# Performance work log

Hardware: AMD Instinct MI355X
Metric: run time of the kernel (lower is better)

Reference implementation:

```python
import jax, jax.numpy as jnp
import numpy as np

DEG = 3
KNOTS = np.array([i / 9.0 for i in range(1, 9)], dtype=np.float32)  # 8 knots in (0,1)
SDIM = DEG + 1 + len(KNOTS)  # 12
B, D_IN, D_HID, D_OUT = 32768, 256, 256, 1


def spline_basis(t):
    # TruncatedPowerBasis: [1, t, t^2, t^3, relu(t-k)^3 ...]  -> (B, SDIM)
    powers = t[:, None] ** jnp.arange(DEG + 1, dtype=t.dtype)
    knots = jnp.asarray(KNOTS, dtype=t.dtype)
    spl = jax.nn.relu(t[:, None] - knots[None, :]) ** DEG
    return jnp.concatenate([powers, spl], axis=1)


def vc_layer(x, basis, W, b, in_dim, out_dim):
    # Mathematically identical to torch: W_b = basis @ W (viewed (in,out)); out = x @ W_b + basis @ b
    # Factored to avoid materializing the (B, in, out) per-sample weight tensor.
    Ws = W.reshape(SDIM, in_dim, out_dim)
    tmp = jnp.einsum('bi,sio->bso', x, Ws)        # (B, SDIM, out)
    return jnp.einsum('bs,bso->bo', basis, tmp) + basis @ b


def setup_inputs() -> dict:
    key = jax.random.key(0)
    ks = jax.random.split(key, 8)
    xavier = lambda k, shape: jax.random.uniform(
        k, shape, dtype=jnp.float32,
        minval=-1.0, maxval=1.0) * np.sqrt(6.0 / (shape[0] + shape[1]))
    return {
        'treatment': jax.random.uniform(ks[0], (B,), dtype=jnp.float32),
        'features': jax.random.normal(ks[1], (B, D_IN), dtype=jnp.float32),
        'W0': xavier(ks[2], (SDIM, D_IN * D_HID)),
        'b0': xavier(ks[3], (SDIM, D_HID)),
        'W1': xavier(ks[4], (SDIM, D_HID * D_HID)),
        'b1': xavier(ks[5], (SDIM, D_HID)),
        'W2': xavier(ks[6], (SDIM, D_HID * D_OUT)),
        'b2': xavier(ks[7], (SDIM, D_OUT)),
    }


def reference(treatment, features, W0, b0, W1, b1, W2, b2):
    basis = spline_basis(treatment)                     # (B, SDIM)
    x = vc_layer(features, basis, W0, b0, D_IN, D_HID)
    x = jax.nn.relu(x)
    x = vc_layer(x, basis, W1, b1, D_HID, D_HID)
    x = jax.nn.relu(x)
    x = vc_layer(x, basis, W2, b2, D_HID, D_OUT)        # (B, 1)
    return x
```

## Files before the change

### kernel.cpp

```cpp
#include <hip/hip_runtime.h>


typedef __attribute__((ext_vector_type(8))) _Float16 half8;
typedef __attribute__((ext_vector_type(4))) _Float16 half4;
typedef __attribute__((ext_vector_type(4))) float floatx4;

#define XPAD 264

__device__ __forceinline__ void gload16(const _Float16* g, _Float16* l){
  __builtin_amdgcn_global_load_lds(
      (const __attribute__((address_space(1))) void*)g,
      (__attribute__((address_space(3))) void*)l, 16, 0, 0);
}

__device__ __forceinline__ void stage_b(const _Float16* wt, _Float16* slot,
                                        int w, int l){
  gload16(wt +        w * 512 + l * 8, slot +        w * 512);
  gload16(wt + 4096 + w * 512 + l * 8, slot + 4096 + w * 512);
}

__device__ __forceinline__ void make_basis(float t, float* p){
  p[0] = 1.f; p[1] = t; p[2] = t*t; p[3] = p[2]*t;
  const float knots[8] = {1.f/9.f, 2.f/9.f, 3.f/9.f, 4.f/9.f,
                          5.f/9.f, 6.f/9.f, 7.f/9.f, 8.f/9.f};
  #pragma unroll
  for (int j = 0; j < 8; ++j){
    float d = t - knots[j];
    d = fmaxf(d, 0.f);
    p[4+j] = d*d*d;
  }
}

__global__ __launch_bounds__(256)
void pack_w_kernel(const float* __restrict__ W0, const float* __restrict__ W1,
                   _Float16* __restrict__ Wp0, _Float16* __restrict__ Wp1){
  __shared__ float wl[32 * 260];
  const int blk = blockIdx.x;
  const float* W = (blk < 96) ? W0 : W1;
  _Float16* Wp   = (blk < 96) ? Wp0 : Wp1;
  const int c    = (blk < 96) ? blk : blk - 96;
  const int tid  = threadIdx.x;
  const float* src = W + (size_t)c * 8192;
  #pragma unroll
  for (int it = 0; it < 8; ++it){
    int idx = it * 256 + tid;
    int r = idx >> 6, c4 = idx & 63;
    float4 v = *(const float4*)(src + (size_t)idx * 4);
    float* d = &wl[r * 260 + c4 * 4];
    d[0] = v.x; d[1] = v.y; d[2] = v.z; d[3] = v.w;
  }
  __syncthreads();
  const int tpos = (c & 7) * 12 + (c >> 3);
  _Float16* dst = Wp + (size_t)tpos * 8192;
  #pragma unroll
  for (int w = 0; w < 4; ++w){
    int v = w * 256 + tid;
    int n16 = v & 15, qq = (v >> 4) & 3, ntg = v >> 6;
    half8 o;
    #pragma unroll
    for (int j = 0; j < 8; ++j)
      o[j] = (_Float16)wl[(qq * 8 + j) * 260 + ntg * 16 + n16];
    *(half8*)(dst + (size_t)v * 8) = o;
  }
}

__device__ __forceinline__ void gemm_kloop(const _Float16* Xl, _Float16* Bl,
                                           const float* bldsT,
                                           const _Float16* __restrict__ wp,
                                           unsigned xbase, int wm, int wn,
                                           int l16, int w, int l,
                                           floatx4 acc[4][4]){
  const unsigned bbase = (unsigned)(wn * 2048 + l * 8);
  half8 xc[4], xn[4], bc[4], bn[4];
  stage_b(wp + 2 * 8192, Bl + 2 * 8192, w, l);
  #pragma unroll
  for (int nt = 0; nt < 4; ++nt)
    bc[nt] = *(const half8*)(Bl + bbase + nt * 512);
  #pragma unroll
  for (int mt = 0; mt < 4; ++mt)
    xc[mt] = *(const half8*)&Xl[xbase + mt * 16 * XPAD];
  floatx4 btc = *(const floatx4*)&bldsT[wm * 64 + l16 * 4];

  for (int ko = 0; ko < 8; ++ko){
    #pragma unroll
    for (int s = 0; s < 12; ++s){
      __asm__ __volatile__("s_waitcnt vmcnt(2)" ::: "memory");
      __builtin_amdgcn_sched_barrier(0);
      __builtin_amdgcn_s_barrier();
      __builtin_amdgcn_sched_barrier(0);

      #pragma unroll
      for (int nt = 0; nt < 4; ++nt)
        bn[nt] = *(const half8*)(Bl + ((s + 1) & 3) * 8192 + bbase + nt * 512);
      const int sn = (s == 11) ? 0 : s + 1;
      floatx4 btn = *(const floatx4*)&bldsT[sn * 128 + wm * 64 + l16 * 4];
      if (s == 0){
        const int kon = (ko + 1) & 7;
        #pragma unroll
        for (int mt = 0; mt < 4; ++mt)
          xn[mt] = *(const half8*)&Xl[xbase + kon * 32 + mt * 16 * XPAD];
      }

      _Float16 bh[4];
      #pragma unroll
      for (int mt = 0; mt < 4; ++mt) bh[mt] = (_Float16)btc[mt];
      half8 az[4];
      #pragma unroll
      for (int mt = 0; mt < 4; ++mt) az[mt] = xc[mt] * bh[mt];
      #pragma unroll
      for (int mt = 0; mt < 4; ++mt)
        #pragma unroll
        for (int nt = 0; nt < 4; ++nt)
          acc[mt][nt] = __builtin_amdgcn_mfma_f32_16x16x32_f16(
              az[mt], bc[nt], acc[mt][nt], 0, 0, 0);

      #pragma unroll
      for (int nt = 0; nt < 4; ++nt) bc[nt] = bn[nt];
      btc = btn;
      if (s == 11){
        #pragma unroll
        for (int mt = 0; mt < 4; ++mt) xc[mt] = xn[mt];
      }
      stage_b(wp + (size_t)(ko * 12 + s + 3) * 8192,
              Bl + ((s + 3) & 3) * 8192, w, l);
    }
  }
}

__device__ __forceinline__ void add_bias(const float* blds, const float* __restrict__ bias,
                                         int wm, int wn, int q, int l16,
                                         floatx4 acc[4][4]){
  for (int s = 0; s < 12; ++s){
    float bl[4];
    #pragma unroll
    for (int nt = 0; nt < 4; ++nt)
      bl[nt] = bias[s * 256 + wn * 64 + nt * 16 + l16];
    floatx4 bs[4];
    #pragma unroll
    for (int mt = 0; mt < 4; ++mt)
      bs[mt] = *(const floatx4*)&blds[s * 128 + wm * 64 + mt * 16 + q * 4];
    #pragma unroll
    for (int mt = 0; mt < 4; ++mt)
      #pragma unroll
      for (int nt = 0; nt < 4; ++nt)
        #pragma unroll
        for (int r = 0; r < 4; ++r)
          acc[mt][nt][r] += bs[mt][r] * bl[nt];
  }
}

__device__ __forceinline__ void scatter_to_xl(_Float16* Xl, floatx4 acc[4][4],
                                              int wm, int wn, int q, int l16){
  #pragma unroll
  for (int mt = 0; mt < 4; ++mt)
    #pragma unroll
    for (int nt = 0; nt < 4; ++nt)
      #pragma unroll
      for (int r = 0; r < 4; ++r)
        Xl[(wm * 64 + mt * 16 + q * 4 + r) * XPAD + wn * 64 + nt * 16 + l16] =
            (_Float16)fmaxf(acc[mt][nt][r], 0.f);
}

__global__ __launch_bounds__(512, 2)
void fused_layers_kernel(const float* __restrict__ feat, const float* __restrict__ treat,
                         const _Float16* __restrict__ Wp0, const float* __restrict__ b0,
                         const _Float16* __restrict__ Wp1, const float* __restrict__ b1,
                         _Float16* __restrict__ X2){
  __shared__ _Float16 Xl[128 * XPAD];
  __shared__ _Float16 Bl[4 * 8192];
  __shared__ float blds[12 * 128];
  __shared__ float bldsT[12 * 128];

  const int tid  = threadIdx.x;
  const int m0   = blockIdx.x * 128;
  const int lane = tid & 63;
  const int wid  = tid >> 6;
  const int wm   = wid >> 2;
  const int wn   = wid & 3;
  const int q    = lane >> 4;
  const int l16  = lane & 15;

  stage_b(Wp0,        Bl,        wid, lane);
  stage_b(Wp0 + 8192, Bl + 8192, wid, lane);

  #pragma unroll
  for (int it = 0; it < 16; ++it){
    int idx = it * 512 + tid;
    int m = idx >> 6, c = idx & 63;
    float4 v = *(const float4*)(feat + (size_t)(m0 + m) * 256 + c * 4);
    half4 h = { (_Float16)v.x, (_Float16)v.y, (_Float16)v.z, (_Float16)v.w };
    *(half4*)&Xl[m * XPAD + c * 4] = h;
  }
  if (tid < 128){
    float t = treat[m0 + tid];
    float p[12]; make_basis(t, p);
    const int r   = tid;
    const int tmt = (r >> 4) & 3;
    const int tl  = r & 15;
    const int twm = r >> 6;
    #pragma unroll
    for (int s = 0; s < 12; ++s){
      blds [s * 128 + r] = p[s];
      bldsT[s * 128 + twm * 64 + tl * 4 + tmt] = p[s];
    }
  }
  __syncthreads();

  const unsigned xbase = (unsigned)(wm * 64 + l16) * XPAD + q * 8;

  const floatx4 zero = {0.f, 0.f, 0.f, 0.f};
  floatx4 acc[4][4];
  #pragma unroll
  for (int mt = 0; mt < 4; ++mt)
    #pragma unroll
    for (int nt = 0; nt < 4; ++nt) acc[mt][nt] = zero;

  gemm_kloop(Xl, Bl, bldsT, Wp0, xbase, wm, wn, l16, wid, lane, acc);
  add_bias(blds, b0, wm, wn, q, l16, acc);
  __syncthreads();
  scatter_to_xl(Xl, acc, wm, wn, q, l16);
  stage_b(Wp1,        Bl,        wid, lane);
  stage_b(Wp1 + 8192, Bl + 8192, wid, lane);
  __syncthreads();

  #pragma unroll
  for (int mt = 0; mt < 4; ++mt)
    #pragma unroll
    for (int nt = 0; nt < 4; ++nt) acc[mt][nt] = zero;
  gemm_kloop(Xl, Bl, bldsT, Wp1, xbase, wm, wn, l16, wid, lane, acc);
  add_bias(blds, b1, wm, wn, q, l16, acc);

  __syncthreads();
  scatter_to_xl(Xl, acc, wm, wn, q, l16);
  __syncthreads();
  #pragma unroll
  for (int it = 0; it < 8; ++it){
    int idx = it * 512 + tid;
    int m = idx >> 5, c = idx & 31;
    half8 v = *(const half8*)&Xl[m * XPAD + c * 8];
    *(half8*)(X2 + (size_t)(m0 + m) * 256 + c * 8) = v;
  }
}

__global__ __launch_bounds__(256)
void final_kernel(const _Float16* __restrict__ X2, const float* __restrict__ treat,
                  const float* __restrict__ W2, const float* __restrict__ b2,
                  float* __restrict__ out){
  __shared__ float w2l[12 * 256];
  __shared__ float b2l[12];
  const int tid = threadIdx.x;
  const int m0 = blockIdx.x * 16;
  #pragma unroll
  for (int it = 0; it < 12; ++it) w2l[it * 256 + tid] = W2[it * 256 + tid];
  if (tid < 12) b2l[tid] = b2[tid];
  __syncthreads();
  const int lane = tid & 63, wid = tid >> 6;
  #pragma unroll
  for (int rr = 0; rr < 4; ++rr){
    int b = m0 + wid * 4 + rr;
    float t = treat[b];
    float p[12]; make_basis(t, p);
    half4 xv = *(const half4*)(X2 + (size_t)b * 256 + lane * 4);
    float xs[4] = { (float)xv.x, (float)xv.y, (float)xv.z, (float)xv.w };
    float ws[4] = {0.f, 0.f, 0.f, 0.f};
    #pragma unroll
    for (int s = 0; s < 12; ++s){
      floatx4 w4 = *(const floatx4*)&w2l[s * 256 + lane * 4];
      #pragma unroll
      for (int j = 0; j < 4; ++j) ws[j] += p[s] * w4[j];
    }
    float dot = xs[0]*ws[0] + xs[1]*ws[1] + xs[2]*ws[2] + xs[3]*ws[3];
    #pragma unroll
    for (int off = 32; off > 0; off >>= 1) dot += __shfl_down(dot, off, 64);
    if (lane == 0){
      float bb = 0.f;
      #pragma unroll
      for (int s = 0; s < 12; ++s) bb += p[s] * b2l[s];
      out[b] = dot + bb;
    }
  }
}

extern "C" void kernel_launch(void* const* d_in, const int* in_sizes, int n_in,
                              void* d_out, int out_size, void* d_ws, size_t ws_size,
                              hipStream_t stream){
  const float* treat = (const float*)d_in[0];
  const float* feat  = (const float*)d_in[1];
  const float* W0    = (const float*)d_in[2];
  const float* b0    = (const float*)d_in[3];
  const float* W1    = (const float*)d_in[4];
  const float* b1    = (const float*)d_in[5];
  const float* W2    = (const float*)d_in[6];
  const float* b2    = (const float*)d_in[7];

  char* ws = (char*)d_ws;
  _Float16* Wp0 = (_Float16*)(ws);
  _Float16* Wp1 = (_Float16*)(ws + 1572864);
  _Float16* X2  = (_Float16*)(ws + 3145728);
  float* out = (float*)d_out;

  pack_w_kernel<<<192, 256, 0, stream>>>(W0, W1, Wp0, Wp1);
  fused_layers_kernel<<<256, 512, 0, stream>>>(feat, treat, Wp0, b0, Wp1, b1, X2);
  final_kernel<<<2048, 256, 0, stream>>>(X2, treat, W2, b2, out);
}
```

Measured before the change: 186.1 us.

## Fuse final layer into main kernel, prefetch B earlier, raise MFMA priority

Folds the third varying-coefficient layer (output dim 1) into the fused two-layer kernel. The ReLU'd layer-1 accumulators are reduced in registers against W2 and the basis, then combined with shuffles and a small LDS buffer. This removes the fp16 X2 round trip through global memory and one kernel launch. It also issues the next B-tile staging load before the MFMA block instead of after it, and wraps the MFMAs in s_setprio. The trade-off is extra LDS for w2l and redbuf, which may affect the 2-blocks-per-CU occupancy, and more register pressure at the kernel tail.

```diff
diff --git a/kernel.cpp b/kernel.cpp
--- a/kernel.cpp
+++ b/kernel.cpp
@@ -100,6 +100,8 @@
         for (int mt = 0; mt < 4; ++mt)
           xn[mt] = *(const half8*)&Xl[xbase + kon * 32 + mt * 16 * XPAD];
       }
+      stage_b(wp + (size_t)(ko * 12 + s + 3) * 8192,
+              Bl + ((s + 3) & 3) * 8192, w, l);
 
       _Float16 bh[4];
       #pragma unroll
@@ -107,12 +109,14 @@
       half8 az[4];
       #pragma unroll
       for (int mt = 0; mt < 4; ++mt) az[mt] = xc[mt] * bh[mt];
+      __builtin_amdgcn_s_setprio(1);
       #pragma unroll
       for (int mt = 0; mt < 4; ++mt)
         #pragma unroll
         for (int nt = 0; nt < 4; ++nt)
           acc[mt][nt] = __builtin_amdgcn_mfma_f32_16x16x32_f16(
               az[mt], bc[nt], acc[mt][nt], 0, 0, 0);
+      __builtin_amdgcn_s_setprio(0);
 
       #pragma unroll
       for (int nt = 0; nt < 4; ++nt) bc[nt] = bn[nt];
@@ -121,8 +125,6 @@
         #pragma unroll
         for (int mt = 0; mt < 4; ++mt) xc[mt] = xn[mt];
       }
-      stage_b(wp + (size_t)(ko * 12 + s + 3) * 8192,
-              Bl + ((s + 3) & 3) * 8192, w, l);
     }
   }
 }
@@ -162,14 +164,18 @@
 }
 
 __global__ __launch_bounds__(512, 2)
-void fused_layers_kernel(const float* __restrict__ feat, const float* __restrict__ treat,
-                         const _Float16* __restrict__ Wp0, const float* __restrict__ b0,
-                         const _Float16* __restrict__ Wp1, const float* __restrict__ b1,
-                         _Float16* __restrict__ X2){
+void fused_all_kernel(const float* __restrict__ feat, const float* __restrict__ treat,
+                      const _Float16* __restrict__ Wp0, const float* __restrict__ b0,
+                      const _Float16* __restrict__ Wp1, const float* __restrict__ b1,
+                      const float* __restrict__ W2, const float* __restrict__ b2,
+                      float* __restrict__ out){
   __shared__ _Float16 Xl[128 * XPAD];
   __shared__ _Float16 Bl[4 * 8192];
   __shared__ float blds[12 * 128];
   __shared__ float bldsT[12 * 128];
+  __shared__ float w2l[12 * 256];
+  __shared__ float redbuf[128 * 4];
+  __shared__ float b2l[12];
 
   const int tid  = threadIdx.x;
   const int m0   = blockIdx.x * 128;
@@ -191,6 +197,10 @@
     half4 h = { (_Float16)v.x, (_Float16)v.y, (_Float16)v.z, (_Float16)v.w };
     *(half4*)&Xl[m * XPAD + c * 4] = h;
   }
+  #pragma unroll
+  for (int it = 0; it < 6; ++it)
+    w2l[it * 512 + tid] = W2[it * 512 + tid];
+  if (tid < 12) b2l[tid] = b2[tid];
   if (tid < 128){
     float t = treat[m0 + tid];
     float p[12]; make_basis(t, p);
@@ -230,54 +240,64 @@
   gemm_kloop(Xl, Bl, bldsT, Wp1, xbase, wm, wn, l16, wid, lane, acc);
   add_bias(blds, b1, wm, wn, q, l16, acc);
 
-  __syncthreads();
-  scatter_to_xl(Xl, acc, wm, wn, q, l16);
-  __syncthreads();
-  #pragma unroll
-  for (int it = 0; it < 8; ++it){
-    int idx = it * 512 + tid;
-    int m = idx >> 5, c = idx & 31;
-    half8 v = *(const half8*)&Xl[m * XPAD + c * 8];
-    *(half8*)(X2 + (size_t)(m0 + m) * 256 + c * 8) = v;
-  }
-}
-
-__global__ __launch_bounds__(256)
-void final_kernel(const _Float16* __restrict__ X2, const float* __restrict__ treat,
-                  const float* __restrict__ W2, const float* __restrict__ b2,
-                  float* __restrict__ out){
-  __shared__ float w2l[12 * 256];
-  __shared__ float b2l[12];
-  const int tid = threadIdx.x;
-  const int m0 = blockIdx.x * 16;
-  #pragma unroll
-  for (int it = 0; it < 12; ++it) w2l[it * 256 + tid] = W2[it * 256 + tid];
-  if (tid < 12) b2l[tid] = b2[tid];
-  __syncthreads();
-  const int lane = tid & 63, wid = tid >> 6;
-  #pragma unroll
-  for (int rr = 0; rr < 4; ++rr){
-    int b = m0 + wid * 4 + rr;
-    float t = treat[b];
-    float p[12]; make_basis(t, p);
-    half4 xv = *(const half4*)(X2 + (size_t)b * 256 + lane * 4);
-    float xs[4] = { (float)xv.x, (float)xv.y, (float)xv.z, (float)xv.w };
-    float ws[4] = {0.f, 0.f, 0.f, 0.f};
-    #pragma unroll
-    for (int s = 0; s < 12; ++s){
-      floatx4 w4 = *(const floatx4*)&w2l[s * 256 + lane * 4];
-      #pragma unroll
-      for (int j = 0; j < 4; ++j) ws[j] += p[s] * w4[j];
+  #pragma unroll
+  for (int mt = 0; mt < 4; ++mt)
+    #pragma unroll
+    for (int nt = 0; nt < 4; ++nt)
+      #pragma unroll
+      for (int r = 0; r < 4; ++r)
+        acc[mt][nt][r] = fmaxf(acc[mt][nt][r], 0.f);
+  float outp[4][4];
+  #pragma unroll
+  for (int mt = 0; mt < 4; ++mt)
+    #pragma unroll
+    for (int r = 0; r < 4; ++r) outp[mt][r] = 0.f;
+  for (int s = 0; s < 12; ++s){
+    float w2v[4];
+    #pragma unroll
+    for (int nt = 0; nt < 4; ++nt)
+      w2v[nt] = w2l[s * 256 + wn * 64 + nt * 16 + l16];
+    floatx4 bs[4];
+    #pragma unroll
+    for (int mt = 0; mt < 4; ++mt)
+      bs[mt] = *(const floatx4*)&blds[s * 128 + wm * 64 + mt * 16 + q * 4];
+    #pragma unroll
+    for (int mt = 0; mt < 4; ++mt)
+      #pragma unroll
+      for (int r = 0; r < 4; ++r){
+        float tmp = acc[mt][0][r] * w2v[0] + acc[mt][1][r] * w2v[1]
+                  + acc[mt][2][r] * w2v[2] + acc[mt][3][r] * w2v[3];
+        outp[mt][r] += bs[mt][r] * tmp;
+      }
+  }
+  #pragma unroll
+  for (int mt = 0; mt < 4; ++mt)
+    #pragma unroll
+    for (int r = 0; r < 4; ++r){
+      float v = outp[mt][r];
+      v += __shfl_xor(v, 1, 64);
+      v += __shfl_xor(v, 2, 64);
+      v += __shfl_xor(v, 4, 64);
+      v += __shfl_xor(v, 8, 64);
+      outp[mt][r] = v;
     }
-    float dot = xs[0]*ws[0] + xs[1]*ws[1] + xs[2]*ws[2] + xs[3]*ws[3];
-    #pragma unroll
-    for (int off = 32; off > 0; off >>= 1) dot += __shfl_down(dot, off, 64);
-    if (lane == 0){
-      float bb = 0.f;
-      #pragma unroll
-      for (int s = 0; s < 12; ++s) bb += p[s] * b2l[s];
-      out[b] = dot + bb;
-    }
+  if (l16 == 0){
+    #pragma unroll
+    for (int mt = 0; mt < 4; ++mt)
+      #pragma unroll
+      for (int r = 0; r < 4; ++r){
+        int row = wm * 64 + mt * 16 + q * 4 + r;
+        redbuf[row * 4 + wn] = outp[mt][r];
+      }
+  }
+  __syncthreads();
+  if (tid < 128){
+    float v = redbuf[tid * 4 + 0] + redbuf[tid * 4 + 1]
+            + redbuf[tid * 4 + 2] + redbuf[tid * 4 + 3];
+    float bb = 0.f;
+    #pragma unroll
+    for (int s = 0; s < 12; ++s) bb += blds[s * 128 + tid] * b2l[s];
+    out[m0 + tid] = v + bb;
   }
 }
 
@@ -296,10 +316,9 @@
   char* ws = (char*)d_ws;
   _Float16* Wp0 = (_Float16*)(ws);
   _Float16* Wp1 = (_Float16*)(ws + 1572864);
-  _Float16* X2  = (_Float16*)(ws + 3145728);
   float* out = (float*)d_out;
 
   pack_w_kernel<<<192, 256, 0, stream>>>(W0, W1, Wp0, Wp1);
-  fused_layers_kernel<<<256, 512, 0, stream>>>(feat, treat, Wp0, b0, Wp1, b1, X2);
-  final_kernel<<<2048, 256, 0, stream>>>(X2, treat, W2, b2, out);
-}
+  fused_all_kernel<<<256, 512, 0, stream>>>(feat, treat, Wp0, b0, Wp1, b1,
+                                            W2, b2, out);
+}
```

Measured after the change: 188.3 us. Within noise of the previous version (+1.2%).
